# Performance work log

Measured on AMD Instinct MI355X. Metric: run time of the kernel, lower is better.

## Reference

```python
import jax, jax.numpy as jnp
import numpy as np

B, IN, OUT = 128, 1024, 1024
BETA, THRESHOLD, RESET = 0.99, 1.0, 0.8
TAU_POS, TAU_NEG = 20.0, 20.0
A_POS, A_NEG = 0.005, 0.005


def setup_inputs() -> dict:
    key = jax.random.key(0)
    k1, k2, k3, k4, k5 = jax.random.split(key, 5)
    in_spikes = (jax.random.uniform(k1, (B, IN)) < 0.1).astype(jnp.float32)
    # nn.Linear default init: U(-1/sqrt(in), 1/sqrt(in))
    bound = 1.0 / np.sqrt(IN)
    W = jax.random.uniform(k2, (OUT, IN), minval=-bound, maxval=bound, dtype=jnp.float32)
    membrane = jax.random.normal(k3, (B, OUT), dtype=jnp.float32) * 0.5
    # trace timers (time since last spike), random in [0, 50)
    delta_pre = jax.random.uniform(k4, (B, IN), dtype=jnp.float32) * 50.0
    delta_fire = jax.random.uniform(k5, (B, OUT), dtype=jnp.float32) * 50.0
    return {"in_spikes": in_spikes, "W": W, "membrane": membrane,
            "delta_pre": delta_pre, "delta_fire": delta_fire}


def reference(in_spikes, W, membrane, delta_pre, delta_fire):
    # dense projection (bias is unused in the original forward)
    weighted = jnp.matmul(in_spikes, W.T)                      # (B, OUT)
    # LIF neuron
    mem = membrane * BETA + weighted
    spike = (mem > THRESHOLD).astype(jnp.float32)
    mem = jnp.where(spike > 0, mem - RESET, mem)
    # trace updates: increment, reset-to-zero where a spike occurred
    dp = jnp.where(in_spikes > 0, 0.0, delta_pre + 1.0)        # (B, IN)
    df = jnp.where(spike > 0, 0.0, delta_fire + 1.0)           # (B, OUT)
    # pairwise timing difference: (B, IN, OUT)
    delta_t = df[:, None, :] - dp[:, :, None]
    potentiation = (delta_t > 0) * (A_POS * jnp.exp(-delta_t / TAU_POS))
    depression = (delta_t < 0) * (A_NEG * jnp.exp(delta_t / TAU_NEG))
    weight_changes = potentiation - depression                 # (B, IN, OUT)
    avg_weight_changes = weight_changes.mean(axis=0).T         # (OUT, IN)
    new_W = W + avg_weight_changes
    return spike, new_W, mem
```

## Files before the change

### kernel.cpp

```cpp
#include <hip/hip_runtime.h>
#include <cstdint>
#include <cmath>

#define Bb   128
#define INN  1024
#define OUTN 1024
#define A_TOT   (0.005f / 128.0f)
#define INV_TAU (1.0f / 20.0f)

__device__ __forceinline__ uint32_t rne_bf16(float f) {
    uint32_t u = __float_as_uint(f);
    return (u + 0x7fffu + ((u >> 16) & 1u)) >> 16;
}

__global__ __launch_bounds__(256) void prep_k(
    const float* __restrict__ W, const float* __restrict__ in_spikes,
    const float* __restrict__ delta_pre,
    float* __restrict__ Wt, uint32_t* __restrict__ IPackB,
    int* __restrict__ gIdx, int* __restrict__ gCount) {
    __shared__ float tile[32][33];
    const int blk = blockIdx.x;
    const int t   = threadIdx.x;

    if ((blk & 3) == 0 && t < 64) {
        const int b = blk >> 2;
        int base = 0;
#pragma unroll
        for (int c = 0; c < 16; c++) {
            float s = in_spikes[(size_t)b * INN + c * 64 + t];
            unsigned long long m = __ballot(s > 0.0f);
            if (s > 0.0f) {
                int pos = base + __popcll(m & ((1ULL << t) - 1ULL));
                gIdx[b * INN + pos] = c * 64 + t;
            }
            base += __popcll(m);
        }
        if (t == 0) gCount[b] = base;
    }

    {
        const int e = blk * 256 + t;
        float sp = in_spikes[e];
        float dp = (sp > 0.0f) ? 0.0f : delta_pre[e] + 1.0f;
        float Iz = expf(-dp * INV_TAU);
        float Iy = A_TOT * expf(dp * INV_TAU);
        IPackB[e] = (rne_bf16(Iz) << 16) | rne_bf16(Iy);
    }

    const int x = t & 31, y = t >> 5;
#pragma unroll
    for (int k = 0; k < 2; k++) {
        int tau = blk * 2 + k;
        int bx = tau & 31, by = tau >> 5;
        __syncthreads();
#pragma unroll
        for (int j = 0; j < 4; j++)
            tile[y + j * 8][x] = W[(size_t)(by * 32 + y + j * 8) * INN + bx * 32 + x];
        __syncthreads();
#pragma unroll
        for (int j = 0; j < 4; j++)
            Wt[(size_t)(bx * 32 + y + j * 8) * OUTN + by * 32 + x] = tile[x][y + j * 8];
    }
}

__global__ __launch_bounds__(256) void spmv_lif_k(
    const float* __restrict__ Wt, const float* __restrict__ membrane,
    const float* __restrict__ delta_fire,
    const int* __restrict__ gIdx, const int* __restrict__ gCount,
    uint32_t* __restrict__ OPackT,
    float* __restrict__ out_spike, float* __restrict__ out_mem) {
    __shared__ int sIdx[INN];
    const int b = blockIdx.x;
    const int z = blockIdx.y;
    const int t = threadIdx.x;
    const int n = gCount[b];
    for (int j = t; j < n; j += 256) sIdx[j] = gIdx[b * INN + j];
    __syncthreads();

    const int o = z * 256 + t;
    float acc = 0.0f;
    int j = 0;
    for (; j + 8 <= n; j += 8) {
        float w0 = Wt[(size_t)sIdx[j + 0] * OUTN + o];
        float w1 = Wt[(size_t)sIdx[j + 1] * OUTN + o];
        float w2 = Wt[(size_t)sIdx[j + 2] * OUTN + o];
        float w3 = Wt[(size_t)sIdx[j + 3] * OUTN + o];
        float w4 = Wt[(size_t)sIdx[j + 4] * OUTN + o];
        float w5 = Wt[(size_t)sIdx[j + 5] * OUTN + o];
        float w6 = Wt[(size_t)sIdx[j + 6] * OUTN + o];
        float w7 = Wt[(size_t)sIdx[j + 7] * OUTN + o];
        acc += ((w0 + w1) + (w2 + w3)) + ((w4 + w5) + (w6 + w7));
    }
    for (; j < n; j++) acc += Wt[(size_t)sIdx[j] * OUTN + o];

    const int n_bo = b * OUTN + o;
    float mem = membrane[n_bo] * 0.99f + acc;
    float s = (mem > 1.0f) ? 1.0f : 0.0f;
    mem = (s > 0.0f) ? mem - 0.8f : mem;
    out_spike[n_bo] = s;
    out_mem[n_bo] = mem;

    float df = (s > 0.0f) ? 0.0f : delta_fire[n_bo] + 1.0f;
    float Oy = expf(-df * INV_TAU);
    float Oz = -A_TOT * expf(df * INV_TAU);
    OPackT[(size_t)o * Bb + b] = (rne_bf16(Oy) << 16) | rne_bf16(Oz);
}

__global__ __launch_bounds__(256, 2) void stdp_k(
    const float* __restrict__ W, const uint32_t* __restrict__ OPackT,
    const uint32_t* __restrict__ IPackB, float* __restrict__ outW) {
    __shared__ uint32_t sOT[32 * 32];
    __shared__ uint32_t sI[32 * 64];
    const int t  = threadIdx.x;
    const int o0 = blockIdx.x * 32;
    const int i0 = blockIdx.y * 64;
    const int tx = t & 15;
    const int ty = t >> 4;
    const int swz = ty & 7;

    float acc[2][4] = {{0.f, 0.f, 0.f, 0.f}, {0.f, 0.f, 0.f, 0.f}};

    for (int cb = 0; cb < Bb / 32; cb++) {
        const int b0 = cb * 32;
        {
            const int col = t & 31, rbase = t >> 5;
#pragma unroll
            for (int r = 0; r < 4; r++) {
                const int orow = r * 8 + rbase;
                const uint32_t v = OPackT[(size_t)(o0 + orow) * Bb + b0 + col];
                sOT[orow * 32 + ((((col >> 2) ^ ((orow >> 1) & 7)) << 2) | (col & 3))] = v;
            }
        }
#pragma unroll
        for (int r = 0; r < 2; r++) {
            const int idx = r * 256 + t;
            const int row = idx >> 4, col = (idx & 15) * 4;
            *(uint4*)&sI[row * 64 + col] =
                *(const uint4*)&IPackB[(size_t)(b0 + row) * INN + i0 + col];
        }
        __syncthreads();

#pragma unroll
        for (int c4 = 0; c4 < 8; c4++) {
            const int chunk = (c4 ^ swz) << 2;
            uint4 oA = *(const uint4*)&sOT[(2 * ty + 0) * 32 + chunk];
            uint4 oB = *(const uint4*)&sOT[(2 * ty + 1) * 32 + chunk];
            const uint32_t ovA[4] = {oA.x, oA.y, oA.z, oA.w};
            const uint32_t ovB[4] = {oB.x, oB.y, oB.z, oB.w};
#pragma unroll
            for (int k = 0; k < 4; k++) {
                uint4 pi = *(const uint4*)&sI[(4 * c4 + k) * 64 + 4 * tx];
                const uint32_t iv[4] = {pi.x, pi.y, pi.z, pi.w};
#pragma unroll
                for (int c = 0; c < 4; c++) {
                    uint32_t k0 = min(ovA[k], iv[c]);
                    uint32_t p0 = max(ovA[k], iv[c]) << 16;
                    acc[0][c] = fmaf(__uint_as_float(k0),
                                     __uint_as_float(p0), acc[0][c]);
                    uint32_t k1 = min(ovB[k], iv[c]);
                    uint32_t p1 = max(ovB[k], iv[c]) << 16;
                    acc[1][c] = fmaf(__uint_as_float(k1),
                                     __uint_as_float(p1), acc[1][c]);
                }
            }
        }
        __syncthreads();
    }

#pragma unroll
    for (int a = 0; a < 2; a++) {
        const size_t off = (size_t)(o0 + 2 * ty + a) * INN + i0 + 4 * tx;
        float4 w = *(const float4*)&W[off];
        *(float4*)&outW[off] = make_float4(w.x + acc[a][0], w.y + acc[a][1],
                                           w.z + acc[a][2], w.w + acc[a][3]);
    }
}

extern "C" void kernel_launch(void* const* d_in, const int* in_sizes, int n_in,
                              void* d_out, int out_size, void* d_ws, size_t ws_size,
                              hipStream_t stream) {
    const float* in_spikes  = (const float*)d_in[0];
    const float* W          = (const float*)d_in[1];
    const float* membrane   = (const float*)d_in[2];
    const float* delta_pre  = (const float*)d_in[3];
    const float* delta_fire = (const float*)d_in[4];

    float* out_spike = (float*)d_out;
    float* out_W     = out_spike + (size_t)Bb * OUTN;
    float* out_mem   = out_W + (size_t)OUTN * INN;

    float* ws        = (float*)d_ws;
    float* Wt        = ws;
    uint32_t* OPackT = (uint32_t*)(Wt + (size_t)INN * OUTN);
    uint32_t* IPackB = OPackT + (size_t)OUTN * Bb;
    int* gIdx        = (int*)(IPackB + (size_t)Bb * INN);
    int* gCount      = gIdx + (size_t)Bb * INN;

    hipLaunchKernelGGL(prep_k, dim3(512), dim3(256), 0, stream,
                       W, in_spikes, delta_pre, Wt, IPackB, gIdx, gCount);
    hipLaunchKernelGGL(spmv_lif_k, dim3(Bb, 4), dim3(256), 0, stream,
                       Wt, membrane, delta_fire, gIdx, gCount,
                       OPackT, out_spike, out_mem);
    hipLaunchKernelGGL(stdp_k, dim3(OUTN / 32, INN / 64), dim3(256), 0, stream,
                       W, OPackT, IPackB, out_W);
}
```

Baseline: 102.0 us.

## Transpose input-trace pack and shrink STDP tiles to 32x32 with 2x2 outputs

```diff
diff --git a/kernel.cpp b/kernel.cpp
--- a/kernel.cpp
+++ b/kernel.cpp
@@ -16,7 +16,7 @@
 __global__ __launch_bounds__(256) void prep_k(
     const float* __restrict__ W, const float* __restrict__ in_spikes,
     const float* __restrict__ delta_pre,
-    float* __restrict__ Wt, uint32_t* __restrict__ IPackB,
+    float* __restrict__ Wt, uint32_t* __restrict__ IPackT,
     int* __restrict__ gIdx, int* __restrict__ gCount) {
     __shared__ float tile[32][33];
     const int blk = blockIdx.x;
@@ -40,11 +40,12 @@
 
     {
         const int e = blk * 256 + t;
+        const int b = e >> 10, i = e & 1023;
         float sp = in_spikes[e];
         float dp = (sp > 0.0f) ? 0.0f : delta_pre[e] + 1.0f;
         float Iz = expf(-dp * INV_TAU);
         float Iy = A_TOT * expf(dp * INV_TAU);
-        IPackB[e] = (rne_bf16(Iz) << 16) | rne_bf16(Iy);
+        IPackT[(size_t)i * Bb + b] = (rne_bf16(Iz) << 16) | rne_bf16(Iy);
     }
 
     const int x = t & 31, y = t >> 5;
@@ -106,73 +107,71 @@
     OPackT[(size_t)o * Bb + b] = (rne_bf16(Oy) << 16) | rne_bf16(Oz);
 }
 
-__global__ __launch_bounds__(256, 2) void stdp_k(
+__global__ __launch_bounds__(256, 4) void stdp_k(
     const float* __restrict__ W, const uint32_t* __restrict__ OPackT,
-    const uint32_t* __restrict__ IPackB, float* __restrict__ outW) {
+    const uint32_t* __restrict__ IPackT, float* __restrict__ outW) {
     __shared__ uint32_t sOT[32 * 32];
-    __shared__ uint32_t sI[32 * 64];
+    __shared__ uint32_t sIT[32 * 32];
     const int t  = threadIdx.x;
     const int o0 = blockIdx.x * 32;
-    const int i0 = blockIdx.y * 64;
+    const int i0 = blockIdx.y * 32;
     const int tx = t & 15;
     const int ty = t >> 4;
-    const int swz = ty & 7;
-
-    float acc[2][4] = {{0.f, 0.f, 0.f, 0.f}, {0.f, 0.f, 0.f, 0.f}};
+    const int srow = t >> 3;
+    const int sc   = t & 7;
+    const int swr  = (srow >> 1) & 7;
+    const int so = ty & 7, si = tx & 7;
+
+    float acc[2][2] = {{0.f, 0.f}, {0.f, 0.f}};
 
     for (int cb = 0; cb < Bb / 32; cb++) {
         const int b0 = cb * 32;
-        {
-            const int col = t & 31, rbase = t >> 5;
-#pragma unroll
-            for (int r = 0; r < 4; r++) {
-                const int orow = r * 8 + rbase;
-                const uint32_t v = OPackT[(size_t)(o0 + orow) * Bb + b0 + col];
-                sOT[orow * 32 + ((((col >> 2) ^ ((orow >> 1) & 7)) << 2) | (col & 3))] = v;
+        *(uint4*)&sOT[srow * 32 + ((sc ^ swr) << 2)] =
+            *(const uint4*)&OPackT[(size_t)(o0 + srow) * Bb + b0 + 4 * sc];
+        *(uint4*)&sIT[srow * 32 + ((sc ^ swr) << 2)] =
+            *(const uint4*)&IPackT[(size_t)(i0 + srow) * Bb + b0 + 4 * sc];
+        __syncthreads();
+
+#pragma unroll
+        for (int c4 = 0; c4 < 8; c4++) {
+            const int co = (c4 ^ so) << 2;
+            const int ci = (c4 ^ si) << 2;
+            uint4 oA = *(const uint4*)&sOT[(2 * ty + 0) * 32 + co];
+            uint4 oB = *(const uint4*)&sOT[(2 * ty + 1) * 32 + co];
+            uint4 iA = *(const uint4*)&sIT[(2 * tx + 0) * 32 + ci];
+            uint4 iB = *(const uint4*)&sIT[(2 * tx + 1) * 32 + ci];
+            const uint32_t ovA[4] = {oA.x, oA.y, oA.z, oA.w};
+            const uint32_t ovB[4] = {oB.x, oB.y, oB.z, oB.w};
+            const uint32_t ivA[4] = {iA.x, iA.y, iA.z, iA.w};
+            const uint32_t ivB[4] = {iB.x, iB.y, iB.z, iB.w};
+#pragma unroll
+            for (int k = 0; k < 4; k++) {
+                uint32_t k00 = min(ovA[k], ivA[k]);
+                uint32_t p00 = max(ovA[k], ivA[k]) << 16;
+                acc[0][0] = fmaf(__uint_as_float(k00), __uint_as_float(p00),
+                                 acc[0][0]);
+                uint32_t k01 = min(ovA[k], ivB[k]);
+                uint32_t p01 = max(ovA[k], ivB[k]) << 16;
+                acc[0][1] = fmaf(__uint_as_float(k01), __uint_as_float(p01),
+                                 acc[0][1]);
+                uint32_t k10 = min(ovB[k], ivA[k]);
+                uint32_t p10 = max(ovB[k], ivA[k]) << 16;
+                acc[1][0] = fmaf(__uint_as_float(k10), __uint_as_float(p10),
+                                 acc[1][0]);
+                uint32_t k11 = min(ovB[k], ivB[k]);
+                uint32_t p11 = max(ovB[k], ivB[k]) << 16;
+                acc[1][1] = fmaf(__uint_as_float(k11), __uint_as_float(p11),
+                                 acc[1][1]);
             }
         }
-#pragma unroll
-        for (int r = 0; r < 2; r++) {
-            const int idx = r * 256 + t;
-            const int row = idx >> 4, col = (idx & 15) * 4;
-            *(uint4*)&sI[row * 64 + col] =
-                *(const uint4*)&IPackB[(size_t)(b0 + row) * INN + i0 + col];
-        }
-        __syncthreads();
-
-#pragma unroll
-        for (int c4 = 0; c4 < 8; c4++) {
-            const int chunk = (c4 ^ swz) << 2;
-            uint4 oA = *(const uint4*)&sOT[(2 * ty + 0) * 32 + chunk];
-            uint4 oB = *(const uint4*)&sOT[(2 * ty + 1) * 32 + chunk];
-            const uint32_t ovA[4] = {oA.x, oA.y, oA.z, oA.w};
-            const uint32_t ovB[4] = {oB.x, oB.y, oB.z, oB.w};
-#pragma unroll
-            for (int k = 0; k < 4; k++) {
-                uint4 pi = *(const uint4*)&sI[(4 * c4 + k) * 64 + 4 * tx];
-                const uint32_t iv[4] = {pi.x, pi.y, pi.z, pi.w};
-#pragma unroll
-                for (int c = 0; c < 4; c++) {
-                    uint32_t k0 = min(ovA[k], iv[c]);
-                    uint32_t p0 = max(ovA[k], iv[c]) << 16;
-                    acc[0][c] = fmaf(__uint_as_float(k0),
-                                     __uint_as_float(p0), acc[0][c]);
-                    uint32_t k1 = min(ovB[k], iv[c]);
-                    uint32_t p1 = max(ovB[k], iv[c]) << 16;
-                    acc[1][c] = fmaf(__uint_as_float(k1),
-                                     __uint_as_float(p1), acc[1][c]);
-                }
-            }
-        }
         __syncthreads();
     }
 
 #pragma unroll
     for (int a = 0; a < 2; a++) {
-        const size_t off = (size_t)(o0 + 2 * ty + a) * INN + i0 + 4 * tx;
-        float4 w = *(const float4*)&W[off];
-        *(float4*)&outW[off] = make_float4(w.x + acc[a][0], w.y + acc[a][1],
-                                           w.z + acc[a][2], w.w + acc[a][3]);
+        const size_t off = (size_t)(o0 + 2 * ty + a) * INN + i0 + 2 * tx;
+        float2 w = *(const float2*)&W[off];
+        *(float2*)&outW[off] = make_float2(w.x + acc[a][0], w.y + acc[a][1]);
     }
 }
 
@@ -192,15 +191,15 @@
     float* ws        = (float*)d_ws;
     float* Wt        = ws;
     uint32_t* OPackT = (uint32_t*)(Wt + (size_t)INN * OUTN);
-    uint32_t* IPackB = OPackT + (size_t)OUTN * Bb;
-    int* gIdx        = (int*)(IPackB + (size_t)Bb * INN);
+    uint32_t* IPackT = OPackT + (size_t)OUTN * Bb;
+    int* gIdx        = (int*)(IPackT + (size_t)INN * Bb);
     int* gCount      = gIdx + (size_t)Bb * INN;
 
     hipLaunchKernelGGL(prep_k, dim3(512), dim3(256), 0, stream,
-                       W, in_spikes, delta_pre, Wt, IPackB, gIdx, gCount);
+                       W, in_spikes, delta_pre, Wt, IPackT, gIdx, gCount);
     hipLaunchKernelGGL(spmv_lif_k, dim3(Bb, 4), dim3(256), 0, stream,
                        Wt, membrane, delta_fire, gIdx, gCount,
                        OPackT, out_spike, out_mem);
-    hipLaunchKernelGGL(stdp_k, dim3(OUTN / 32, INN / 64), dim3(256), 0, stream,
-                       W, OPackT, IPackB, out_W);
-}
+    hipLaunchKernelGGL(stdp_k, dim3(OUTN / 32, INN / 32), dim3(256), 0, stream,
+                       W, OPackT, IPackT, out_W);
+}
```

Measured after the change: 99.93 us, median of 2. 2.0% less time.
